# Kernel optimization log

Hardware: AMD Instinct MI355X
Metric: run time of the kernel (lower is better)

The kernel has to match this reference:

```python
import jax, jax.numpy as jnp
import numpy as np

B, P, K, L, F, KS, NCLS = 8, 4096, 20, 10, 32, 5, 40
N = B * P


def setup_inputs() -> dict:
    key = jax.random.key(0)
    k = jax.random.split(key, 5)
    return {
        "pos": jax.random.normal(k[0], (N, 3), jnp.float32),
        "Wsp": jax.random.normal(k[1], (KS ** 3, F), jnp.float32) * 0.1,
        "root": jax.random.normal(k[2], (F,), jnp.float32) * 0.1,
        "bias": jnp.zeros((F,), jnp.float32),
        "gamma": jnp.ones((F,), jnp.float32),
        "beta": jnp.zeros((F,), jnp.float32),
        "W1": jax.random.normal(k[3], (F, 256), jnp.float32) * 0.1,
        "b1": jnp.zeros((256,), jnp.float32),
        "W2": jax.random.normal(k[4], (256, NCLS), jnp.float32) * 0.1,
        "b2": jnp.zeros((NCLS,), jnp.float32),
    }


def _knn(pos):
    # per-graph brute-force knn (loop=False), neighbors sorted by distance
    pts = pos.reshape(B, P, 3)

    def one(p):
        d = jnp.sum((p[:, None, :] - p[None, :, :]) ** 2, -1)  # (P,P)
        d = d.at[jnp.arange(P), jnp.arange(P)].set(jnp.inf)
        return jax.lax.top_k(-d, K)[1]

    nbr = jax.vmap(one)(pts) + (jnp.arange(B) * P)[:, None, None]
    return nbr.reshape(N, K)


def _eig3(A):
    # power iteration with deflation (nr_iterations=5) on batched 3x3 symmetric mats
    def pi(M):
        v = jnp.full((M.shape[0], 3), np.float32(3.0 ** -0.5))
        for _ in range(5):
            v = jnp.einsum("nij,nj->ni", M, v)
            v = v / (jnp.linalg.norm(v, axis=-1, keepdims=True) + 1e-12)
        lam = jnp.einsum("ni,nij,nj->n", v, M, v)
        return lam, v

    l1, v1 = pi(A)
    _, v2 = pi(A - l1[:, None, None] * v1[:, :, None] * v1[:, None, :])
    v3 = jnp.cross(v1, v2)
    v3 = v3 / (jnp.linalg.norm(v3, axis=-1, keepdims=True) + 1e-12)
    return jnp.stack([v1, v2, v3], axis=1)  # rows = eigenvectors, V[:,2] = normal


def reference(pos, Wsp, root, bias, gamma, beta, W1, b1, W2, b2):
    nbr = _knn(pos)                               # (N,K)
    clusters = pos[nbr] - pos[:, None, :]         # (N,K,3) neighbor - center
    cov = jnp.einsum("nmc,nmd->ncd", clusters[:, :L], clusters[:, :L])
    V = _eig3(cov)                                # (N,3,3)
    dirc = jnp.einsum("nkc,ndc->nkd", clusters, V)  # clusters @ V^T
    signs = jnp.sign(dirc[:, :, 2].sum(1))
    dirc = dirc.at[:, :, 2].multiply(signs[:, None])
    max_abs = jnp.max(jnp.abs(dirc).reshape(N, -1), 1)
    dirc = dirc / max_abs[:, None, None] * 0.5 + 0.5  # pseudo coords in [0,1]

    # SplineConv, degree=1, open splines, dim=3, in_channels=1 (x=ones)
    v = dirc * (KS - 1)
    f = jnp.floor(v)
    frac = v - f
    fi = f.astype(jnp.int32)
    bits = jnp.array([[(s >> 2) & 1, (s >> 1) & 1, s & 1] for s in range(8)], jnp.int32)
    idx = jnp.clip(fi[:, :, None, :] + bits[None, None, :, :], 0, KS - 1)  # (N,K,8,3)
    wgt = jnp.where(bits[None, None] == 1, frac[:, :, None, :], 1.0 - frac[:, :, None, :])
    basis = wgt.prod(-1)                                          # (N,K,8)
    flat = (idx[..., 0] * KS + idx[..., 1]) * KS + idx[..., 2]    # (N,K,8)
    msg = jnp.einsum("nks,nksf->nf", basis, Wsp[flat]) / K        # mean aggregation
    node = msg + root + bias                                      # root weight on x=1

    # BatchNorm1d (training-mode batch stats, eps=1e-5)
    mu = node.mean(0)
    var = ((node - mu) ** 2).mean(0)
    xb = gamma * (node - mu) / jnp.sqrt(var + 1e-5) + beta

    out3 = xb[:, :, None] * V[:, 2][:, None, :]   # (N,F,3) scale normal direction
    y = jax.nn.sigmoid(out3)
    ys = y.reshape(-1, P, F).mean(1)              # (3B,F) as in torch .view
    y1 = jax.nn.elu(ys @ W1 + b1)
    return jax.nn.log_softmax(y1 @ W2 + b2, axis=1)
```

## Files before the change

kernel.cpp:

```cpp
#include <hip/hip_runtime.h>
#include <hip/hip_bf16.h>
#include <math.h>

#define BGR 8
#define PP 4096
#define NPTS 32768
#define KNN 20
#define LCOV 10
#define FF 32
#define KS 5
#define NCLS 40
#define NGROUP 24
#define GROUPLEN 131072

#define SPLIT 8
#define CHUNK (PP / SPLIT)
#define PTSBLK 128
#define KTHR 1024
#define CAP 7
#define NSLOT (KNN + 1)
#define MPAD NSLOT
#define SENT 0xFFFFFFFFu
#define NSAMP 48

__device__ inline unsigned umn(unsigned a, unsigned b) { return a < b ? a : b; }
__device__ inline unsigned umx(unsigned a, unsigned b) { return a > b ? a : b; }

__device__ inline void mat3vec(const float M[9], const float v[3], float w[3]) {
    w[0] = M[0] * v[0] + M[1] * v[1] + M[2] * v[2];
    w[1] = M[3] * v[0] + M[4] * v[1] + M[5] * v[2];
    w[2] = M[6] * v[0] + M[7] * v[1] + M[8] * v[2];
}

__device__ inline float pi3(const float M[9], float v[3]) {
    v[0] = v[1] = v[2] = 0.57735026918962576f;
#pragma unroll
    for (int it = 0; it < 5; ++it) {
        float w[3];
        mat3vec(M, v, w);
        float nrm = sqrtf(w[0] * w[0] + w[1] * w[1] + w[2] * w[2]) + 1e-12f;
        v[0] = w[0] / nrm;
        v[1] = w[1] / nrm;
        v[2] = w[2] / nrm;
    }
    float w[3];
    mat3vec(M, v, w);
    return v[0] * w[0] + v[1] * w[1] + v[2] * w[2];
}

#define SCELLS 4096
__global__ __launch_bounds__(1024) void sort_kernel(
    const float* __restrict__ pos, unsigned short* __restrict__ perm) {
    __shared__ unsigned cnt[SCELLS];
    __shared__ unsigned short cellOf[PP];
    __shared__ unsigned tsum[1024];
    int g = blockIdx.x;
    int tid = threadIdx.x;
    const float* gp = pos + (size_t)g * PP * 3;
    for (int i = tid; i < SCELLS; i += 1024) cnt[i] = 0;
    __syncthreads();
    for (int i = tid; i < PP; i += 1024) {
        float x = gp[i * 3 + 0];
        float y = gp[i * 3 + 1];
        float z = gp[i * 3 + 2];
        int cx = min(max((int)floorf((x + 4.0f) * 2.0f), 0), 15);
        int cy = min(max((int)floorf((y + 4.0f) * 2.0f), 0), 15);
        int cz = min(max((int)floorf((z + 4.0f) * 2.0f), 0), 15);
        unsigned m = 0;
#pragma unroll
        for (int bb = 0; bb < 4; ++bb)
            m |= (((unsigned)(cx >> bb) & 1u) << (3 * bb + 2)) |
                 (((unsigned)(cy >> bb) & 1u) << (3 * bb + 1)) |
                 (((unsigned)(cz >> bb) & 1u) << (3 * bb + 0));
        cellOf[i] = (unsigned short)m;
        atomicAdd(&cnt[m], 1u);
    }
    __syncthreads();
    unsigned c0 = cnt[4 * tid + 0];
    unsigned c1 = cnt[4 * tid + 1];
    unsigned c2 = cnt[4 * tid + 2];
    unsigned c3 = cnt[4 * tid + 3];
    unsigned local = c0 + c1 + c2 + c3;
    tsum[tid] = local;
    __syncthreads();
    for (int off = 1; off < 1024; off <<= 1) {
        unsigned v = (tid >= off) ? tsum[tid - off] : 0u;
        __syncthreads();
        tsum[tid] += v;
        __syncthreads();
    }
    unsigned base = tsum[tid] - local;
    cnt[4 * tid + 0] = base;
    cnt[4 * tid + 1] = base + c0;
    cnt[4 * tid + 2] = base + c0 + c1;
    cnt[4 * tid + 3] = base + c0 + c1 + c2;
    __syncthreads();
    for (int i = tid; i < PP; i += 1024) {
        unsigned dst = atomicAdd(&cnt[cellOf[i]], 1u);
        perm[g * PP + dst] = (unsigned short)i;
    }
}

__global__ __launch_bounds__(KTHR, 8) void knn_kernel(
    const float* __restrict__ pos, const unsigned short* __restrict__ perm,
    unsigned short* __restrict__ nbr16, float* __restrict__ Rbuf,
    float* __restrict__ v3out) {
    __shared__ float smem[4 * PP];
    __shared__ unsigned samp[PTSBLK * 24];
    __shared__ float Tseed[PTSBLK];
    __shared__ unsigned short sli[PTSBLK];
    float* tx = smem;
    float* ty = smem + PP;
    float* tz = smem + 2 * PP;
    float* tw = smem + 3 * PP;
    unsigned short* lnbr = (unsigned short*)(smem + 3 * PP + 2816);

    int b = blockIdx.x >> 5;
    int blkInGraph = blockIdx.x & 31;
    const float* gp = pos + (size_t)b * PP * 3;
    if (threadIdx.x < PTSBLK)
        sli[threadIdx.x] = perm[b * PP + blkInGraph * PTSBLK + threadIdx.x];
    for (int i = threadIdx.x; i < PP; i += KTHR) {
        float x = gp[i * 3 + 0];
        float y = gp[i * 3 + 1];
        float z = gp[i * 3 + 2];
        tx[i] = -2.0f * x;
        ty[i] = -2.0f * y;
        tz[i] = -2.0f * z;
        tw[i] = x * x + y * y + z * z;
    }
    __syncthreads();

    int eighth = threadIdx.x >> 7;
    int pt = threadIdx.x & (PTSBLK - 1);
    int li = sli[pt];
    float px = -0.5f * tx[li];
    float py = -0.5f * ty[li];
    float pz = -0.5f * tz[li];
    float p2 = tw[li];
    int jbeg = eighth * CHUNK;

    {
        unsigned s0 = SENT, s1 = SENT, s2 = SENT;
        for (int jj = jbeg; jj < jbeg + NSAMP; ++jj) {
            float dh = fmaf(px, tx[jj], fmaf(py, ty[jj], fmaf(pz, tz[jj], tw[jj])));
            float d = fmaxf(dh + p2, 0.0f);
            unsigned key = (__float_as_uint(d) & 0xFFFFF000u) | (unsigned)jj;
            if (jj == li) key = SENT;
            unsigned t0 = umn(key, s0); key = umx(key, s0); s0 = t0;
            t0 = umn(key, s1); key = umx(key, s1); s1 = t0;
            s2 = umn(key, s2);
        }
        unsigned* sdst = &samp[pt * 24 + eighth * 3];
        sdst[0] = s0; sdst[1] = s1; sdst[2] = s2;
    }
    __syncthreads();
    if (threadIdx.x < PTSBLK) {
        unsigned g0 = 0, g1 = 0, g2 = 0, g3 = 0;
        const unsigned* ss = &samp[threadIdx.x * 24];
#pragma unroll
        for (int i = 0; i < 24; ++i) {
            unsigned k = ss[i], a;
            a = umx(k, g0); k = umn(k, g0); g0 = a;
            a = umx(k, g1); k = umn(k, g1); g1 = a;
            a = umx(k, g2); k = umn(k, g2); g2 = a;
            g3 = umx(k, g3);
        }
        Tseed[threadIdx.x] = __uint_as_float((g3 & 0xFFFFF000u) + 0x2000u);
    }
    __syncthreads();
    float seed_hat = Tseed[pt] - p2;

    unsigned bd[NSLOT];
#pragma unroll
    for (int k = 0; k < NSLOT; k++) bd[k] = SENT;
    float worst_hat = seed_hat;

    unsigned bufk[CAP];
#pragma unroll
    for (int s = 0; s < CAP; s++) bufk[s] = SENT;

    auto flush = [&]() {
#pragma unroll
        for (int s = 0; s < CAP; s++) {
            if (!__any(bufk[s] != SENT)) break;
            unsigned k = bufk[s];
#pragma unroll
            for (int i = 0; i < NSLOT; i++) {
                unsigned lo = umn(k, bd[i]);
                k = umx(k, bd[i]);
                bd[i] = lo;
            }
            bufk[s] = SENT;
        }
        unsigned wb = bd[NSLOT - 1];
        float nw = (wb == SENT) ? INFINITY
                                : __uint_as_float(wb & 0xFFFFF000u) - p2;
        worst_hat = fminf(nw, seed_hat);
    };

    for (int jj = jbeg; jj < jbeg + CHUNK; jj += 4) {
        float4 xv = *(const float4*)(tx + jj);
        float4 yv = *(const float4*)(ty + jj);
        float4 zv = *(const float4*)(tz + jj);
        float4 wv = *(const float4*)(tw + jj);
        float xa[4] = {xv.x, xv.y, xv.z, xv.w};
        float ya[4] = {yv.x, yv.y, yv.z, yv.w};
        float za[4] = {zv.x, zv.y, zv.z, zv.w};
        float wa[4] = {wv.x, wv.y, wv.z, wv.w};
#pragma unroll
        for (int u = 0; u < 4; u++) {
            float dh = fmaf(px, xa[u], fmaf(py, ya[u], fmaf(pz, za[u], wa[u])));
            if (dh < worst_hat) {
                float d = fmaxf(dh + p2, 0.0f);
                unsigned key = (__float_as_uint(d) & 0xFFFFF000u)
                               | (unsigned)(jj + u);
                bufk[6] = bufk[5];
                bufk[5] = bufk[4];
                bufk[4] = bufk[3];
                bufk[3] = bufk[2];
                bufk[2] = bufk[1];
                bufk[1] = bufk[0];
                bufk[0] = key;
            }
        }
        if (__any(bufk[3] != SENT)) flush();
    }
    flush();

    __syncthreads();
    unsigned* mk = (unsigned*)smem;
    for (int h = 0; h < 2; h++) {
        if ((pt >> 6) == h) {
            int lpt = pt & 63;
#pragma unroll
            for (int k = 0; k < NSLOT; k++)
                mk[(eighth * 64 + lpt) * MPAD + k] = bd[k];
        }
        __syncthreads();
        if (threadIdx.x < 64) {
            int p = threadIdx.x;
            const unsigned* base = &mk[p * MPAD];
            int cur[SPLIT];
#pragma unroll
            for (int q = 0; q < SPLIT; q++) cur[q] = 0;
            int lpt2 = h * 64 + p;
            int gi = b * PP + (int)sli[lpt2];
#pragma unroll
            for (int t = 0; t < NSLOT; t++) {
                unsigned v[SPLIT];
#pragma unroll
                for (int q = 0; q < SPLIT; q++)
                    v[q] = base[q * 64 * MPAD + cur[q]];
                unsigned m = v[0];
#pragma unroll
                for (int q = 1; q < SPLIT; q++) m = umn(m, v[q]);
                if (t > 0) {
                    int local = (int)(m & 0xFFFu);
                    nbr16[(size_t)gi * KNN + (t - 1)] = (unsigned short)local;
                    lnbr[lpt2 * KNN + (t - 1)] = (unsigned short)local;
                }
#pragma unroll
                for (int q = 0; q < SPLIT; q++) cur[q] += (v[q] == m);
            }
        }
        __syncthreads();
    }

    for (int i = threadIdx.x; i < PP; i += KTHR) {
        tx[i] = gp[i * 3 + 0];
        ty[i] = gp[i * 3 + 1];
        tz[i] = gp[i * 3 + 2];
    }
    __syncthreads();

    if (threadIdx.x < PTSBLK) {
        int lp = threadIdx.x;
        int ng = sli[lp];
        int n = b * PP + ng;
        float qx = tx[ng], qy = ty[ng], qz = tz[ng];
        const unsigned short* ln = &lnbr[lp * KNN];

        float m00 = 0.f, m01 = 0.f, m02 = 0.f, m11 = 0.f, m12 = 0.f, m22 = 0.f;
#pragma unroll
        for (int k = 0; k < LCOV; k++) {
            int id = ln[k];
            float cx = tx[id] - qx;
            float cy = ty[id] - qy;
            float cz = tz[id] - qz;
            m00 += cx * cx; m01 += cx * cy; m02 += cx * cz;
            m11 += cy * cy; m12 += cy * cz; m22 += cz * cz;
        }
        float M[9] = {m00, m01, m02, m01, m11, m12, m02, m12, m22};

        float v1[3], v2[3], v3[3];
        float l1 = pi3(M, v1);
        float M2[9];
#pragma unroll
        for (int c = 0; c < 3; c++)
#pragma unroll
            for (int d = 0; d < 3; d++)
                M2[c * 3 + d] = M[c * 3 + d] - l1 * v1[c] * v1[d];
        pi3(M2, v2);
        v3[0] = v1[1] * v2[2] - v1[2] * v2[1];
        v3[1] = v1[2] * v2[0] - v1[0] * v2[2];
        v3[2] = v1[0] * v2[1] - v1[1] * v2[0];
        {
            float nrm = sqrtf(v3[0] * v3[0] + v3[1] * v3[1] + v3[2] * v3[2]) + 1e-12f;
            v3[0] /= nrm; v3[1] /= nrm; v3[2] /= nrm;
        }

        float ssum = 0.f, mx = 0.f;
#pragma unroll
        for (int k = 0; k < KNN; k++) {
            int id = ln[k];
            float cx = tx[id] - qx;
            float cy = ty[id] - qy;
            float cz = tz[id] - qz;
            float d0 = cx * v1[0] + cy * v1[1] + cz * v1[2];
            float d1 = cx * v2[0] + cy * v2[1] + cz * v2[2];
            float d2 = cx * v3[0] + cy * v3[1] + cz * v3[2];
            ssum += d2;
            mx = fmaxf(mx, fabsf(d0));
            mx = fmaxf(mx, fabsf(d1));
            mx = fmaxf(mx, fabsf(d2));
        }
        float sgn = (ssum > 0.f) ? 1.f : ((ssum < 0.f) ? -1.f : 0.f);

        float sc = 2.0f / mx;
        float* R = Rbuf + (size_t)n * 12;
        R[0] = v1[0] * sc;  R[1] = v1[1] * sc;  R[2] = v1[2] * sc;
        R[3] = v2[0] * sc;  R[4] = v2[1] * sc;  R[5] = v2[2] * sc;
        float s2 = sgn * sc;
        R[6] = v3[0] * s2;  R[7] = v3[1] * s2;  R[8] = v3[2] * s2;
        R[9] = 0.f; R[10] = 0.f; R[11] = 0.f;

        v3out[n * 3 + 0] = v3[0];
        v3out[n * 3 + 1] = v3[1];
        v3out[n * 3 + 2] = v3[2];
    }
}

#define NPB 16
#define SPLBLKS (NPTS / NPB)
__global__ __launch_bounds__(512) void spline_kernel(
    const float* __restrict__ pos, const unsigned short* __restrict__ nbr16,
    const float* __restrict__ Rbuf, const float* __restrict__ Wsp,
    const float* __restrict__ root, const float* __restrict__ bias,
    float* __restrict__ node, float* __restrict__ sums_part) {
    __shared__ float wbuf[NPB * KNN * 8];

    int tid = threadIdx.x;
    if (tid < NPB * KNN) {
        int pt = tid / KNN;
        int k = tid - pt * KNN;
        int n = blockIdx.x * NPB + pt;
        const float4* Rv = (const float4*)(Rbuf + (size_t)n * 12);
        float4 r0 = Rv[0], r1 = Rv[1], r2 = Rv[2];
        float px = pos[n * 3 + 0], py = pos[n * 3 + 1], pz = pos[n * 3 + 2];
        int id = (n & ~(PP - 1)) | (int)nbr16[(size_t)n * KNN + k];
        float cxx = pos[id * 3 + 0] - px;
        float cyy = pos[id * 3 + 1] - py;
        float czz = pos[id * 3 + 2] - pz;
        float v0 = fmaf(cxx, r0.x, fmaf(cyy, r0.y, fmaf(czz, r0.z, 2.0f)));
        float v1 = fmaf(cxx, r0.w, fmaf(cyy, r1.x, fmaf(czz, r1.y, 2.0f)));
        float v2 = fmaf(cxx, r1.z, fmaf(cyy, r1.w, fmaf(czz, r2.x, 2.0f)));
        float f0 = floorf(v0), f1 = floorf(v1), f2 = floorf(v2);
        float fr0 = v0 - f0, fr1 = v1 - f1, fr2 = v2 - f2;
        int fi0 = (int)f0, fi1 = (int)f1, fi2 = (int)f2;
        float* wdst = &wbuf[(pt * KNN + k) * 8];
#pragma unroll
        for (int s = 0; s < 8; s++) {
            int b0 = (s >> 2) & 1, b1 = (s >> 1) & 1, b2s = s & 1;
            int i0 = min(max(fi0 + b0, 0), KS - 1);
            int i1 = min(max(fi1 + b1, 0), KS - 1);
            int i2 = min(max(fi2 + b2s, 0), KS - 1);
            float w = (b0 ? fr0 : 1.f - fr0) * (b1 ? fr1 : 1.f - fr1) *
                      (b2s ? fr2 : 1.f - fr2);
            unsigned flat = (unsigned)((i0 * KS + i1) * KS + i2);
            wdst[s] = __uint_as_float((__float_as_uint(w) & ~127u) | flat);
        }
    }
    __syncthreads();

    int pt = tid >> 5;
    int f = tid & 31;
    const float* wrow = &wbuf[pt * (KNN * 8)];
    float acc = 0.f;
#pragma unroll
    for (int k = 0; k < KNN; k++) {
        float4 wa = *(const float4*)&wrow[k * 8];
        float4 wb = *(const float4*)&wrow[k * 8 + 4];
        float wv[8] = {wa.x, wa.y, wa.z, wa.w, wb.x, wb.y, wb.z, wb.w};
#pragma unroll
        for (int s = 0; s < 8; s++) {
            unsigned u = __float_as_uint(wv[s]) & 127u;
            acc = fmaf(wv[s], Wsp[u * FF + f], acc);
        }
    }
    int n = blockIdx.x * NPB + pt;
    float val = acc * (1.0f / KNN) + root[f] + bias[f];
    node[(size_t)n * FF + f] = val;

    __syncthreads();
    wbuf[tid] = val;
    wbuf[512 + tid] = val * val;
    __syncthreads();
    if (tid < 64) {
        int ff = tid & 31;
        int off = (tid >> 5) * 512;
        float s = 0.f;
#pragma unroll
        for (int p = 0; p < NPB; p++) s += wbuf[off + p * 32 + ff];
        sums_part[(size_t)blockIdx.x * 64 + tid] = s;
    }
}

#define YSPLIT 8
#define YCHUNK (GROUPLEN / YSPLIT)
__global__ __launch_bounds__(256) void ys_kernel(
    const float* __restrict__ node, const float* __restrict__ v3,
    const float* __restrict__ sums_part, const float* __restrict__ gamma,
    const float* __restrict__ beta, float* __restrict__ ys_part) {
    __shared__ float stat4[256];
    __shared__ float stat[64];
    __shared__ float sa[FF], sb[FF];
    {
        int col = threadIdx.x & 63;
        int q = threadIdx.x >> 6;
        float s0 = 0.f, s1 = 0.f, s2 = 0.f, s3 = 0.f;
        for (int p = q * 512; p < (q + 1) * 512; p += 4) {
            s0 += sums_part[(p + 0) * 64 + col];
            s1 += sums_part[(p + 1) * 64 + col];
            s2 += sums_part[(p + 2) * 64 + col];
            s3 += sums_part[(p + 3) * 64 + col];
        }
        stat4[threadIdx.x] = (s0 + s1) + (s2 + s3);
    }
    __syncthreads();
    if (threadIdx.x < 64) {
        stat[threadIdx.x] = stat4[threadIdx.x] + stat4[64 + threadIdx.x] +
                            stat4[128 + threadIdx.x] + stat4[192 + threadIdx.x];
    }
    __syncthreads();
    if (threadIdx.x < FF) {
        int f = threadIdx.x;
        float mu = stat[f] * (1.0f / NPTS);
        float var = stat[FF + f] * (1.0f / NPTS) - mu * mu;
        float inv = 1.0f / sqrtf(var + 1e-5f);
        sa[f] = gamma[f] * inv;
        sb[f] = beta[f] - gamma[f] * inv * mu;
    }
    __syncthreads();

    int g = blockIdx.x >> 3;
    int sub = blockIdx.x & 7;
    int t0 = g * GROUPLEN + sub * YCHUNK + threadIdx.x;
    int n = t0 / 96;
    int r0 = t0 - n * 96;
    int rj[3], fj[3], cj[3], dj[3];
    rj[0] = r0;
    rj[1] = (r0 + 64) % 96;
    rj[2] = (r0 + 32) % 96;
#pragma unroll
    for (int j = 0; j < 3; j++) {
        fj[j] = rj[j] / 3;
        cj[j] = rj[j] - fj[j] * 3;
        dj[j] = (rj[j] >= 32) ? 3 : 2;
    }
    float Sa0 = sa[fj[0]], Sb0 = sb[fj[0]];
    float Sa1 = sa[fj[1]], Sb1 = sb[fj[1]];
    float Sa2 = sa[fj[2]], Sb2 = sb[fj[2]];
    int nf = n * FF;
    int n3 = n * 3;

    float acc = 0.f;
#pragma unroll 1
    for (int tr = 0; tr < 21; tr++) {
        {
            float xb = fmaf(Sa0, node[nf + fj[0]], Sb0);
            float val = xb * v3[n3 + cj[0]];
            acc += 1.0f / (1.0f + __expf(-val));
            nf += dj[0] * FF; n3 += dj[0] * 3;
        }
        {
            float xb = fmaf(Sa1, node[nf + fj[1]], Sb1);
            float val = xb * v3[n3 + cj[1]];
            acc += 1.0f / (1.0f + __expf(-val));
            nf += dj[1] * FF; n3 += dj[1] * 3;
        }
        {
            float xb = fmaf(Sa2, node[nf + fj[2]], Sb2);
            float val = xb * v3[n3 + cj[2]];
            acc += 1.0f / (1.0f + __expf(-val));
            nf += dj[2] * FF; n3 += dj[2] * 3;
        }
    }
    {
        float xb = fmaf(Sa0, node[nf + fj[0]], Sb0);
        float val = xb * v3[n3 + cj[0]];
        acc += 1.0f / (1.0f + __expf(-val));
    }

    __shared__ float red[256];
    red[threadIdx.x] = acc;
    __syncthreads();
    if (threadIdx.x < FF) {
        float s = 0.f;
        for (int t = threadIdx.x; t < 256; t += FF) s += red[t];
        ys_part[(sub * NGROUP + g) * FF + threadIdx.x] = s * (1.0f / PP);
    }
}

__global__ __launch_bounds__(256) void head_kernel(
    const float* __restrict__ ys_part, const float* __restrict__ W1,
    const float* __restrict__ b1, const float* __restrict__ W2,
    const float* __restrict__ b2, float* __restrict__ out) {
    int g = blockIdx.x;
    __shared__ float syr[FF];
    __shared__ float h[256];
    __shared__ float logits[NCLS];
    __shared__ float mstat[2];
    if (threadIdx.x < FF) {
        float s = 0.f;
#pragma unroll
        for (int sub = 0; sub < YSPLIT; sub++)
            s += ys_part[(sub * NGROUP + g) * FF + threadIdx.x];
        syr[threadIdx.x] = s;
    }
    __syncthreads();
    int j = threadIdx.x;
    float acc = b1[j];
#pragma unroll
    for (int f = 0; f < FF; f++) acc += syr[f] * W1[f * 256 + j];
    h[j] = acc > 0.f ? acc : expm1f(acc);
    __syncthreads();
    if (j < NCLS) {
        float l = b2[j];
        for (int q = 0; q < 256; q++) l += h[q] * W2[q * NCLS + j];
        logits[j] = l;
    }
    __syncthreads();
    if (j == 0) {
        float m = -INFINITY;
        for (int o = 0; o < NCLS; o++) m = fmaxf(m, logits[o]);
        float s = 0.f;
        for (int o = 0; o < NCLS; o++) s += expf(logits[o] - m);
        mstat[0] = m;
        mstat[1] = logf(s);
    }
    __syncthreads();
    if (j < NCLS) out[g * NCLS + j] = logits[j] - mstat[0] - mstat[1];
}

extern "C" void kernel_launch(void* const* d_in, const int* in_sizes, int n_in,
                              void* d_out, int out_size, void* d_ws, size_t ws_size,
                              hipStream_t stream) {
    const float* pos   = (const float*)d_in[0];
    const float* Wsp   = (const float*)d_in[1];
    const float* root  = (const float*)d_in[2];
    const float* bias  = (const float*)d_in[3];
    const float* gamma = (const float*)d_in[4];
    const float* beta  = (const float*)d_in[5];
    const float* W1    = (const float*)d_in[6];
    const float* b1    = (const float*)d_in[7];
    const float* W2    = (const float*)d_in[8];
    const float* b2    = (const float*)d_in[9];
    float* out = (float*)d_out;

    char* ws = (char*)d_ws;
    unsigned short* nbr16 = (unsigned short*)(ws);
    float* sums_part = (float*)(ws + 1310720);
    float* ys_part   = (float*)(ws + 1835008);
    unsigned short* perm = (unsigned short*)(ws + 1859584);
    float* node = (float*)(ws + 2621440);
    float* v3   = (float*)(ws + 6815744);
    float* Rbuf = (float*)(ws + 7212288);

    sort_kernel<<<BGR, 1024, 0, stream>>>(pos, perm);
    knn_kernel<<<256, KTHR, 0, stream>>>(pos, perm, nbr16, Rbuf, v3);
    spline_kernel<<<SPLBLKS, 512, 0, stream>>>(pos, nbr16, Rbuf, Wsp, root,
                                               bias, node, sums_part);
    ys_kernel<<<NGROUP * YSPLIT, 256, 0, stream>>>(node, v3, sums_part, gamma,
                                                   beta, ys_part);
    head_kernel<<<NGROUP, 256, 0, stream>>>(ys_part, W1, b1, W2, b2, out);
}
```

Baseline: 224.4 us.

## Fuse Morton sort into kNN and cull point groups by bounding box

```diff
diff --git a/kernel.cpp b/kernel.cpp
--- a/kernel.cpp
+++ b/kernel.cpp
@@ -22,6 +22,8 @@
 #define MPAD NSLOT
 #define SENT 0xFFFFFFFFu
 #define NSAMP 48
+#define SCELLS 4096
+#define NGRP 256
 
 __device__ inline unsigned umn(unsigned a, unsigned b) { return a < b ? a : b; }
 __device__ inline unsigned umx(unsigned a, unsigned b) { return a > b ? a : b; }
@@ -48,67 +50,14 @@
     return v[0] * w[0] + v[1] * w[1] + v[2] * w[2];
 }
 
-#define SCELLS 4096
-__global__ __launch_bounds__(1024) void sort_kernel(
-    const float* __restrict__ pos, unsigned short* __restrict__ perm) {
-    __shared__ unsigned cnt[SCELLS];
-    __shared__ unsigned short cellOf[PP];
-    __shared__ unsigned tsum[1024];
-    int g = blockIdx.x;
-    int tid = threadIdx.x;
-    const float* gp = pos + (size_t)g * PP * 3;
-    for (int i = tid; i < SCELLS; i += 1024) cnt[i] = 0;
-    __syncthreads();
-    for (int i = tid; i < PP; i += 1024) {
-        float x = gp[i * 3 + 0];
-        float y = gp[i * 3 + 1];
-        float z = gp[i * 3 + 2];
-        int cx = min(max((int)floorf((x + 4.0f) * 2.0f), 0), 15);
-        int cy = min(max((int)floorf((y + 4.0f) * 2.0f), 0), 15);
-        int cz = min(max((int)floorf((z + 4.0f) * 2.0f), 0), 15);
-        unsigned m = 0;
-#pragma unroll
-        for (int bb = 0; bb < 4; ++bb)
-            m |= (((unsigned)(cx >> bb) & 1u) << (3 * bb + 2)) |
-                 (((unsigned)(cy >> bb) & 1u) << (3 * bb + 1)) |
-                 (((unsigned)(cz >> bb) & 1u) << (3 * bb + 0));
-        cellOf[i] = (unsigned short)m;
-        atomicAdd(&cnt[m], 1u);
-    }
-    __syncthreads();
-    unsigned c0 = cnt[4 * tid + 0];
-    unsigned c1 = cnt[4 * tid + 1];
-    unsigned c2 = cnt[4 * tid + 2];
-    unsigned c3 = cnt[4 * tid + 3];
-    unsigned local = c0 + c1 + c2 + c3;
-    tsum[tid] = local;
-    __syncthreads();
-    for (int off = 1; off < 1024; off <<= 1) {
-        unsigned v = (tid >= off) ? tsum[tid - off] : 0u;
-        __syncthreads();
-        tsum[tid] += v;
-        __syncthreads();
-    }
-    unsigned base = tsum[tid] - local;
-    cnt[4 * tid + 0] = base;
-    cnt[4 * tid + 1] = base + c0;
-    cnt[4 * tid + 2] = base + c0 + c1;
-    cnt[4 * tid + 3] = base + c0 + c1 + c2;
-    __syncthreads();
-    for (int i = tid; i < PP; i += 1024) {
-        unsigned dst = atomicAdd(&cnt[cellOf[i]], 1u);
-        perm[g * PP + dst] = (unsigned short)i;
-    }
-}
-
-__global__ __launch_bounds__(KTHR, 8) void knn_kernel(
-    const float* __restrict__ pos, const unsigned short* __restrict__ perm,
-    unsigned short* __restrict__ nbr16, float* __restrict__ Rbuf,
-    float* __restrict__ v3out) {
+__global__ __launch_bounds__(KTHR, 4) void knn_kernel(
+    const float* __restrict__ pos, unsigned short* __restrict__ nbr16,
+    float* __restrict__ Rbuf, float* __restrict__ v3out) {
     __shared__ float smem[4 * PP];
+    __shared__ unsigned short mOrig[PP];
     __shared__ unsigned samp[PTSBLK * 24];
     __shared__ float Tseed[PTSBLK];
-    __shared__ unsigned short sli[PTSBLK];
+    __shared__ float4 bbl[NGRP], bbh[NGRP];
     float* tx = smem;
     float* ty = smem + PP;
     float* tz = smem + 2 * PP;
@@ -118,35 +67,103 @@
     int b = blockIdx.x >> 5;
     int blkInGraph = blockIdx.x & 31;
     const float* gp = pos + (size_t)b * PP * 3;
-    if (threadIdx.x < PTSBLK)
-        sli[threadIdx.x] = perm[b * PP + blkInGraph * PTSBLK + threadIdx.x];
-    for (int i = threadIdx.x; i < PP; i += KTHR) {
-        float x = gp[i * 3 + 0];
-        float y = gp[i * 3 + 1];
-        float z = gp[i * 3 + 2];
-        tx[i] = -2.0f * x;
-        ty[i] = -2.0f * y;
-        tz[i] = -2.0f * z;
-        tw[i] = x * x + y * y + z * z;
-    }
-    __syncthreads();
-
-    int eighth = threadIdx.x >> 7;
-    int pt = threadIdx.x & (PTSBLK - 1);
-    int li = sli[pt];
-    float px = -0.5f * tx[li];
-    float py = -0.5f * ty[li];
-    float pz = -0.5f * tz[li];
-    float p2 = tw[li];
+    int tid = threadIdx.x;
+
+    {
+        unsigned* cnt = (unsigned*)smem;
+        unsigned short* cellOf = (unsigned short*)(smem + 4096);
+        unsigned* tsum = (unsigned*)(smem + 6144);
+        for (int i = tid; i < SCELLS; i += KTHR) cnt[i] = 0u;
+        __syncthreads();
+        for (int i = tid; i < PP; i += KTHR) {
+            float x = gp[i * 3 + 0];
+            float y = gp[i * 3 + 1];
+            float z = gp[i * 3 + 2];
+            int cx = min(max((int)floorf((x + 4.0f) * 2.0f), 0), 15);
+            int cy = min(max((int)floorf((y + 4.0f) * 2.0f), 0), 15);
+            int cz = min(max((int)floorf((z + 4.0f) * 2.0f), 0), 15);
+            unsigned m = 0;
+#pragma unroll
+            for (int bb = 0; bb < 4; ++bb)
+                m |= (((unsigned)(cx >> bb) & 1u) << (3 * bb + 2)) |
+                     (((unsigned)(cy >> bb) & 1u) << (3 * bb + 1)) |
+                     (((unsigned)(cz >> bb) & 1u) << (3 * bb + 0));
+            cellOf[i] = (unsigned short)m;
+            atomicAdd(&cnt[m], 1u);
+        }
+        __syncthreads();
+        unsigned c0 = cnt[4 * tid + 0];
+        unsigned c1 = cnt[4 * tid + 1];
+        unsigned c2 = cnt[4 * tid + 2];
+        unsigned c3 = cnt[4 * tid + 3];
+        unsigned local = c0 + c1 + c2 + c3;
+        tsum[tid] = local;
+        __syncthreads();
+        for (int off = 1; off < 1024; off <<= 1) {
+            unsigned v = (tid >= off) ? tsum[tid - off] : 0u;
+            __syncthreads();
+            tsum[tid] += v;
+            __syncthreads();
+        }
+        unsigned base = tsum[tid] - local;
+        cnt[4 * tid + 0] = base;
+        cnt[4 * tid + 1] = base + c0;
+        cnt[4 * tid + 2] = base + c0 + c1;
+        cnt[4 * tid + 3] = base + c0 + c1 + c2;
+        __syncthreads();
+        for (int i = tid; i < PP; i += KTHR) {
+            unsigned dst = atomicAdd(&cnt[cellOf[i]], 1u);
+            mOrig[dst] = (unsigned short)i;
+        }
+    }
+    __syncthreads();
+
+    for (int s = tid; s < PP; s += KTHR) {
+        int oi = mOrig[s];
+        float x = gp[oi * 3 + 0];
+        float y = gp[oi * 3 + 1];
+        float z = gp[oi * 3 + 2];
+        tx[s] = -2.0f * x;
+        ty[s] = -2.0f * y;
+        tz[s] = -2.0f * z;
+        tw[s] = x * x + y * y + z * z;
+    }
+    __syncthreads();
+
+    if (tid < NGRP) {
+        int s0i = tid * 16;
+        float lx = 1e30f, ly = 1e30f, lz = 1e30f;
+        float hx = -1e30f, hy = -1e30f, hz = -1e30f;
+#pragma unroll
+        for (int u = 0; u < 16; ++u) {
+            float rx = -0.5f * tx[s0i + u];
+            float ry = -0.5f * ty[s0i + u];
+            float rz = -0.5f * tz[s0i + u];
+            lx = fminf(lx, rx); hx = fmaxf(hx, rx);
+            ly = fminf(ly, ry); hy = fmaxf(hy, ry);
+            lz = fminf(lz, rz); hz = fmaxf(hz, rz);
+        }
+        bbl[tid] = make_float4(lx, ly, lz, 0.f);
+        bbh[tid] = make_float4(hx, hy, hz, 0.f);
+    }
+
+    int eighth = tid >> 7;
+    int pt = tid & (PTSBLK - 1);
+    int liSlot = blkInGraph * PTSBLK + pt;
+    float px = -0.5f * tx[liSlot];
+    float py = -0.5f * ty[liSlot];
+    float pz = -0.5f * tz[liSlot];
+    float p2 = tw[liSlot];
     int jbeg = eighth * CHUNK;
 
     {
         unsigned s0 = SENT, s1 = SENT, s2 = SENT;
-        for (int jj = jbeg; jj < jbeg + NSAMP; ++jj) {
+        int jj = jbeg;
+        for (int t = 0; t < NSAMP; ++t, jj += 10) {
             float dh = fmaf(px, tx[jj], fmaf(py, ty[jj], fmaf(pz, tz[jj], tw[jj])));
             float d = fmaxf(dh + p2, 0.0f);
             unsigned key = (__float_as_uint(d) & 0xFFFFF000u) | (unsigned)jj;
-            if (jj == li) key = SENT;
+            if (jj == liSlot) key = SENT;
             unsigned t0 = umn(key, s0); key = umx(key, s0); s0 = t0;
             t0 = umn(key, s1); key = umx(key, s1); s1 = t0;
             s2 = umn(key, s2);
@@ -155,9 +172,9 @@
         sdst[0] = s0; sdst[1] = s1; sdst[2] = s2;
     }
     __syncthreads();
-    if (threadIdx.x < PTSBLK) {
+    if (tid < PTSBLK) {
         unsigned g0 = 0, g1 = 0, g2 = 0, g3 = 0;
-        const unsigned* ss = &samp[threadIdx.x * 24];
+        const unsigned* ss = &samp[tid * 24];
 #pragma unroll
         for (int i = 0; i < 24; ++i) {
             unsigned k = ss[i], a;
@@ -166,7 +183,7 @@
             a = umx(k, g2); k = umn(k, g2); g2 = a;
             g3 = umx(k, g3);
         }
-        Tseed[threadIdx.x] = __uint_as_float((g3 & 0xFFFFF000u) + 0x2000u);
+        Tseed[tid] = __uint_as_float((g3 & 0xFFFFF000u) + 0x2000u);
     }
     __syncthreads();
     float seed_hat = Tseed[pt] - p2;
@@ -175,6 +192,7 @@
 #pragma unroll
     for (int k = 0; k < NSLOT; k++) bd[k] = SENT;
     float worst_hat = seed_hat;
+    float td = Tseed[pt];
 
     unsigned bufk[CAP];
 #pragma unroll
@@ -197,34 +215,50 @@
         float nw = (wb == SENT) ? INFINITY
                                 : __uint_as_float(wb & 0xFFFFF000u) - p2;
         worst_hat = fminf(nw, seed_hat);
+        td = worst_hat + p2;
     };
 
-    for (int jj = jbeg; jj < jbeg + CHUNK; jj += 4) {
-        float4 xv = *(const float4*)(tx + jj);
-        float4 yv = *(const float4*)(ty + jj);
-        float4 zv = *(const float4*)(tz + jj);
-        float4 wv = *(const float4*)(tw + jj);
-        float xa[4] = {xv.x, xv.y, xv.z, xv.w};
-        float ya[4] = {yv.x, yv.y, yv.z, yv.w};
-        float za[4] = {zv.x, zv.y, zv.z, zv.w};
-        float wa[4] = {wv.x, wv.y, wv.z, wv.w};
-#pragma unroll
-        for (int u = 0; u < 4; u++) {
-            float dh = fmaf(px, xa[u], fmaf(py, ya[u], fmaf(pz, za[u], wa[u])));
-            if (dh < worst_hat) {
-                float d = fmaxf(dh + p2, 0.0f);
-                unsigned key = (__float_as_uint(d) & 0xFFFFF000u)
-                               | (unsigned)(jj + u);
-                bufk[6] = bufk[5];
-                bufk[5] = bufk[4];
-                bufk[4] = bufk[3];
-                bufk[3] = bufk[2];
-                bufk[2] = bufk[1];
-                bufk[1] = bufk[0];
-                bufk[0] = key;
+    int grp0 = jbeg >> 4;
+#pragma unroll 1
+    for (int grp = 0; grp < CHUNK / 16; ++grp) {
+        float4 bl = bbl[grp0 + grp];
+        float4 bh = bbh[grp0 + grp];
+        float ddx = fmaxf(fmaxf(bl.x - px, px - bh.x), 0.f);
+        float ddy = fmaxf(fmaxf(bl.y - py, py - bh.y), 0.f);
+        float ddz = fmaxf(fmaxf(bl.z - pz, pz - bh.z), 0.f);
+        float m2 = fmaf(ddx, ddx, fmaf(ddy, ddy, ddz * ddz)) * 0.9999f;
+        if (__any(m2 < td)) {
+            int gb = jbeg + (grp << 4);
+#pragma unroll
+            for (int q4 = 0; q4 < 16; q4 += 4) {
+                int jj = gb + q4;
+                float4 xv = *(const float4*)(tx + jj);
+                float4 yv = *(const float4*)(ty + jj);
+                float4 zv = *(const float4*)(tz + jj);
+                float4 wv = *(const float4*)(tw + jj);
+                float xa[4] = {xv.x, xv.y, xv.z, xv.w};
+                float ya[4] = {yv.x, yv.y, yv.z, yv.w};
+                float za[4] = {zv.x, zv.y, zv.z, zv.w};
+                float wa[4] = {wv.x, wv.y, wv.z, wv.w};
+#pragma unroll
+                for (int u = 0; u < 4; u++) {
+                    float dh = fmaf(px, xa[u], fmaf(py, ya[u], fmaf(pz, za[u], wa[u])));
+                    if (dh < worst_hat) {
+                        float d = fmaxf(dh + p2, 0.0f);
+                        unsigned key = (__float_as_uint(d) & 0xFFFFF000u)
+                                       | (unsigned)(jj + u);
+                        bufk[6] = bufk[5];
+                        bufk[5] = bufk[4];
+                        bufk[4] = bufk[3];
+                        bufk[3] = bufk[2];
+                        bufk[2] = bufk[1];
+                        bufk[1] = bufk[0];
+                        bufk[0] = key;
+                    }
+                }
+                if (__any(bufk[3] != SENT)) flush();
             }
         }
-        if (__any(bufk[3] != SENT)) flush();
     }
     flush();
 
@@ -238,14 +272,14 @@
                 mk[(eighth * 64 + lpt) * MPAD + k] = bd[k];
         }
         __syncthreads();
-        if (threadIdx.x < 64) {
-            int p = threadIdx.x;
+        if (tid < 64) {
+            int p = tid;
             const unsigned* base = &mk[p * MPAD];
             int cur[SPLIT];
 #pragma unroll
             for (int q = 0; q < SPLIT; q++) cur[q] = 0;
             int lpt2 = h * 64 + p;
-            int gi = b * PP + (int)sli[lpt2];
+            int gi = b * PP + (int)mOrig[blkInGraph * PTSBLK + lpt2];
 #pragma unroll
             for (int t = 0; t < NSLOT; t++) {
                 unsigned v[SPLIT];
@@ -256,7 +290,7 @@
 #pragma unroll
                 for (int q = 1; q < SPLIT; q++) m = umn(m, v[q]);
                 if (t > 0) {
-                    int local = (int)(m & 0xFFFu);
+                    int local = (int)mOrig[m & 0xFFFu];
                     nbr16[(size_t)gi * KNN + (t - 1)] = (unsigned short)local;
                     lnbr[lpt2 * KNN + (t - 1)] = (unsigned short)local;
                 }
@@ -267,16 +301,16 @@
         __syncthreads();
     }
 
-    for (int i = threadIdx.x; i < PP; i += KTHR) {
+    for (int i = tid; i < PP; i += KTHR) {
         tx[i] = gp[i * 3 + 0];
         ty[i] = gp[i * 3 + 1];
         tz[i] = gp[i * 3 + 2];
     }
     __syncthreads();
 
-    if (threadIdx.x < PTSBLK) {
-        int lp = threadIdx.x;
-        int ng = sli[lp];
+    if (tid < PTSBLK) {
+        int lp = tid;
+        int ng = mOrig[blkInGraph * PTSBLK + lp];
         int n = b * PP + ng;
         float qx = tx[ng], qy = ty[ng], qz = tz[ng];
         const unsigned short* ln = &lnbr[lp * KNN];
@@ -572,13 +606,11 @@
     unsigned short* nbr16 = (unsigned short*)(ws);
     float* sums_part = (float*)(ws + 1310720);
     float* ys_part   = (float*)(ws + 1835008);
-    unsigned short* perm = (unsigned short*)(ws + 1859584);
     float* node = (float*)(ws + 2621440);
     float* v3   = (float*)(ws + 6815744);
     float* Rbuf = (float*)(ws + 7212288);
 
-    sort_kernel<<<BGR, 1024, 0, stream>>>(pos, perm);
-    knn_kernel<<<256, KTHR, 0, stream>>>(pos, perm, nbr16, Rbuf, v3);
+    knn_kernel<<<256, KTHR, 0, stream>>>(pos, nbr16, Rbuf, v3);
     spline_kernel<<<SPLBLKS, 512, 0, stream>>>(pos, nbr16, Rbuf, Wsp, root,
                                                bias, node, sums_part);
     ys_kernel<<<NGROUP * YSPLIT, 256, 0, stream>>>(node, v3, sums_part, gamma,
```

Result: slower. 337.5 us (+50.4%).

## Fuse Morton-sort into knn kernel and seed threshold from sorted-order neighbors

Applied to the files above, without the earlier changes.

```diff
diff --git a/kernel.cpp b/kernel.cpp
--- a/kernel.cpp
+++ b/kernel.cpp
@@ -21,7 +21,7 @@
 #define NSLOT (KNN + 1)
 #define MPAD NSLOT
 #define SENT 0xFFFFFFFFu
-#define NSAMP 48
+#define SCELLS 4096
 
 __device__ inline unsigned umn(unsigned a, unsigned b) { return a < b ? a : b; }
 __device__ inline unsigned umx(unsigned a, unsigned b) { return a > b ? a : b; }
@@ -48,67 +48,13 @@
     return v[0] * w[0] + v[1] * w[1] + v[2] * w[2];
 }
 
-#define SCELLS 4096
-__global__ __launch_bounds__(1024) void sort_kernel(
-    const float* __restrict__ pos, unsigned short* __restrict__ perm) {
-    __shared__ unsigned cnt[SCELLS];
-    __shared__ unsigned short cellOf[PP];
-    __shared__ unsigned tsum[1024];
-    int g = blockIdx.x;
-    int tid = threadIdx.x;
-    const float* gp = pos + (size_t)g * PP * 3;
-    for (int i = tid; i < SCELLS; i += 1024) cnt[i] = 0;
-    __syncthreads();
-    for (int i = tid; i < PP; i += 1024) {
-        float x = gp[i * 3 + 0];
-        float y = gp[i * 3 + 1];
-        float z = gp[i * 3 + 2];
-        int cx = min(max((int)floorf((x + 4.0f) * 2.0f), 0), 15);
-        int cy = min(max((int)floorf((y + 4.0f) * 2.0f), 0), 15);
-        int cz = min(max((int)floorf((z + 4.0f) * 2.0f), 0), 15);
-        unsigned m = 0;
-#pragma unroll
-        for (int bb = 0; bb < 4; ++bb)
-            m |= (((unsigned)(cx >> bb) & 1u) << (3 * bb + 2)) |
-                 (((unsigned)(cy >> bb) & 1u) << (3 * bb + 1)) |
-                 (((unsigned)(cz >> bb) & 1u) << (3 * bb + 0));
-        cellOf[i] = (unsigned short)m;
-        atomicAdd(&cnt[m], 1u);
-    }
-    __syncthreads();
-    unsigned c0 = cnt[4 * tid + 0];
-    unsigned c1 = cnt[4 * tid + 1];
-    unsigned c2 = cnt[4 * tid + 2];
-    unsigned c3 = cnt[4 * tid + 3];
-    unsigned local = c0 + c1 + c2 + c3;
-    tsum[tid] = local;
-    __syncthreads();
-    for (int off = 1; off < 1024; off <<= 1) {
-        unsigned v = (tid >= off) ? tsum[tid - off] : 0u;
-        __syncthreads();
-        tsum[tid] += v;
-        __syncthreads();
-    }
-    unsigned base = tsum[tid] - local;
-    cnt[4 * tid + 0] = base;
-    cnt[4 * tid + 1] = base + c0;
-    cnt[4 * tid + 2] = base + c0 + c1;
-    cnt[4 * tid + 3] = base + c0 + c1 + c2;
-    __syncthreads();
-    for (int i = tid; i < PP; i += 1024) {
-        unsigned dst = atomicAdd(&cnt[cellOf[i]], 1u);
-        perm[g * PP + dst] = (unsigned short)i;
-    }
-}
-
 __global__ __launch_bounds__(KTHR, 8) void knn_kernel(
-    const float* __restrict__ pos, const unsigned short* __restrict__ perm,
-    unsigned short* __restrict__ nbr16, float* __restrict__ Rbuf,
-    float* __restrict__ v3out) {
+    const float* __restrict__ pos, unsigned short* __restrict__ nbr16,
+    float* __restrict__ Rbuf, float* __restrict__ v3out) {
     __shared__ float smem[4 * PP];
+    __shared__ unsigned short mOrig[PP];
     __shared__ unsigned samp[PTSBLK * 24];
     __shared__ float Tseed[PTSBLK];
-    __shared__ unsigned short sli[PTSBLK];
     float* tx = smem;
     float* ty = smem + PP;
     float* tz = smem + 2 * PP;
@@ -118,9 +64,58 @@
     int b = blockIdx.x >> 5;
     int blkInGraph = blockIdx.x & 31;
     const float* gp = pos + (size_t)b * PP * 3;
-    if (threadIdx.x < PTSBLK)
-        sli[threadIdx.x] = perm[b * PP + blkInGraph * PTSBLK + threadIdx.x];
-    for (int i = threadIdx.x; i < PP; i += KTHR) {
+    int tid = threadIdx.x;
+
+    {
+        unsigned* cnt = (unsigned*)smem;
+        unsigned short* cellOf = (unsigned short*)(smem + 4096);
+        unsigned* tsum = (unsigned*)(smem + 6144);
+        for (int i = tid; i < SCELLS; i += KTHR) cnt[i] = 0u;
+        __syncthreads();
+        for (int i = tid; i < PP; i += KTHR) {
+            float x = gp[i * 3 + 0];
+            float y = gp[i * 3 + 1];
+            float z = gp[i * 3 + 2];
+            int cx = min(max((int)floorf((x + 4.0f) * 2.0f), 0), 15);
+            int cy = min(max((int)floorf((y + 4.0f) * 2.0f), 0), 15);
+            int cz = min(max((int)floorf((z + 4.0f) * 2.0f), 0), 15);
+            unsigned m = 0;
+#pragma unroll
+            for (int bb = 0; bb < 4; ++bb)
+                m |= (((unsigned)(cx >> bb) & 1u) << (3 * bb + 2)) |
+                     (((unsigned)(cy >> bb) & 1u) << (3 * bb + 1)) |
+                     (((unsigned)(cz >> bb) & 1u) << (3 * bb + 0));
+            cellOf[i] = (unsigned short)m;
+            atomicAdd(&cnt[m], 1u);
+        }
+        __syncthreads();
+        unsigned c0 = cnt[4 * tid + 0];
+        unsigned c1 = cnt[4 * tid + 1];
+        unsigned c2 = cnt[4 * tid + 2];
+        unsigned c3 = cnt[4 * tid + 3];
+        unsigned local = c0 + c1 + c2 + c3;
+        tsum[tid] = local;
+        __syncthreads();
+        for (int off = 1; off < 1024; off <<= 1) {
+            unsigned v = (tid >= off) ? tsum[tid - off] : 0u;
+            __syncthreads();
+            tsum[tid] += v;
+            __syncthreads();
+        }
+        unsigned base = tsum[tid] - local;
+        cnt[4 * tid + 0] = base;
+        cnt[4 * tid + 1] = base + c0;
+        cnt[4 * tid + 2] = base + c0 + c1;
+        cnt[4 * tid + 3] = base + c0 + c1 + c2;
+        __syncthreads();
+        for (int i = tid; i < PP; i += KTHR) {
+            unsigned dst = atomicAdd(&cnt[cellOf[i]], 1u);
+            mOrig[dst] = (unsigned short)i;
+        }
+    }
+    __syncthreads();
+
+    for (int i = tid; i < PP; i += KTHR) {
         float x = gp[i * 3 + 0];
         float y = gp[i * 3 + 1];
         float z = gp[i * 3 + 2];
@@ -131,9 +126,10 @@
     }
     __syncthreads();
 
-    int eighth = threadIdx.x >> 7;
-    int pt = threadIdx.x & (PTSBLK - 1);
-    int li = sli[pt];
+    int eighth = tid >> 7;
+    int pt = tid & (PTSBLK - 1);
+    int qSlot = blkInGraph * PTSBLK + pt;
+    int li = mOrig[qSlot];
     float px = -0.5f * tx[li];
     float py = -0.5f * ty[li];
     float pz = -0.5f * tz[li];
@@ -141,23 +137,23 @@
     int jbeg = eighth * CHUNK;
 
     {
-        unsigned s0 = SENT, s1 = SENT, s2 = SENT;
-        for (int jj = jbeg; jj < jbeg + NSAMP; ++jj) {
-            float dh = fmaf(px, tx[jj], fmaf(py, ty[jj], fmaf(pz, tz[jj], tw[jj])));
+        int eb = (eighth < 4) ? eighth : (eighth - 4);
+        int sgn = (eighth < 4) ? 1 : -1;
+        unsigned* sdst = &samp[pt * 24 + eighth * 3];
+#pragma unroll
+        for (int i = 0; i < 3; ++i) {
+            int o = sgn * (eb * 3 + i + 1);
+            int s = (qSlot + o) & (PP - 1);
+            int oi = mOrig[s];
+            float dh = fmaf(px, tx[oi], fmaf(py, ty[oi], fmaf(pz, tz[oi], tw[oi])));
             float d = fmaxf(dh + p2, 0.0f);
-            unsigned key = (__float_as_uint(d) & 0xFFFFF000u) | (unsigned)jj;
-            if (jj == li) key = SENT;
-            unsigned t0 = umn(key, s0); key = umx(key, s0); s0 = t0;
-            t0 = umn(key, s1); key = umx(key, s1); s1 = t0;
-            s2 = umn(key, s2);
-        }
-        unsigned* sdst = &samp[pt * 24 + eighth * 3];
-        sdst[0] = s0; sdst[1] = s1; sdst[2] = s2;
-    }
-    __syncthreads();
-    if (threadIdx.x < PTSBLK) {
+            sdst[i] = (__float_as_uint(d) & 0xFFFFF000u) | (unsigned)oi;
+        }
+    }
+    __syncthreads();
+    if (tid < PTSBLK) {
         unsigned g0 = 0, g1 = 0, g2 = 0, g3 = 0;
-        const unsigned* ss = &samp[threadIdx.x * 24];
+        const unsigned* ss = &samp[tid * 24];
 #pragma unroll
         for (int i = 0; i < 24; ++i) {
             unsigned k = ss[i], a;
@@ -166,7 +162,7 @@
             a = umx(k, g2); k = umn(k, g2); g2 = a;
             g3 = umx(k, g3);
         }
-        Tseed[threadIdx.x] = __uint_as_float((g3 & 0xFFFFF000u) + 0x2000u);
+        Tseed[tid] = __uint_as_float((g3 & 0xFFFFF000u) + 0x2000u);
     }
     __syncthreads();
     float seed_hat = Tseed[pt] - p2;
@@ -238,14 +234,14 @@
                 mk[(eighth * 64 + lpt) * MPAD + k] = bd[k];
         }
         __syncthreads();
-        if (threadIdx.x < 64) {
-            int p = threadIdx.x;
+        if (tid < 64) {
+            int p = tid;
             const unsigned* base = &mk[p * MPAD];
             int cur[SPLIT];
 #pragma unroll
             for (int q = 0; q < SPLIT; q++) cur[q] = 0;
             int lpt2 = h * 64 + p;
-            int gi = b * PP + (int)sli[lpt2];
+            int gi = b * PP + (int)mOrig[blkInGraph * PTSBLK + lpt2];
 #pragma unroll
             for (int t = 0; t < NSLOT; t++) {
                 unsigned v[SPLIT];
@@ -267,16 +263,16 @@
         __syncthreads();
     }
 
-    for (int i = threadIdx.x; i < PP; i += KTHR) {
+    for (int i = tid; i < PP; i += KTHR) {
         tx[i] = gp[i * 3 + 0];
         ty[i] = gp[i * 3 + 1];
         tz[i] = gp[i * 3 + 2];
     }
     __syncthreads();
 
-    if (threadIdx.x < PTSBLK) {
-        int lp = threadIdx.x;
-        int ng = sli[lp];
+    if (tid < PTSBLK) {
+        int lp = tid;
+        int ng = mOrig[blkInGraph * PTSBLK + lp];
         int n = b * PP + ng;
         float qx = tx[ng], qy = ty[ng], qz = tz[ng];
         const unsigned short* ln = &lnbr[lp * KNN];
@@ -572,13 +568,11 @@
     unsigned short* nbr16 = (unsigned short*)(ws);
     float* sums_part = (float*)(ws + 1310720);
     float* ys_part   = (float*)(ws + 1835008);
-    unsigned short* perm = (unsigned short*)(ws + 1859584);
     float* node = (float*)(ws + 2621440);
     float* v3   = (float*)(ws + 6815744);
     float* Rbuf = (float*)(ws + 7212288);
 
-    sort_kernel<<<BGR, 1024, 0, stream>>>(pos, perm);
-    knn_kernel<<<256, KTHR, 0, stream>>>(pos, perm, nbr16, Rbuf, v3);
+    knn_kernel<<<256, KTHR, 0, stream>>>(pos, nbr16, Rbuf, v3);
     spline_kernel<<<SPLBLKS, 512, 0, stream>>>(pos, nbr16, Rbuf, Wsp, root,
                                                bias, node, sums_part);
     ys_kernel<<<NGROUP * YSPLIT, 256, 0, stream>>>(node, v3, sums_part, gamma,
```

New measurement: 244.1 us. 1.09x slower.
